# Kernel tuning notes

Hardware: AMD Instinct MI355X
Metric: run time of the kernel (lower is better)

Reference implementation:

```python
import jax, jax.numpy as jnp
import numpy as np
import math

EMB_DIM = 1024
N_HEADS = 16
HEAD_DIM = EMB_DIM // N_HEADS
B, T = 4, 2048


def bitlinear(x, w):
    # BitNet b1.58 absmean ternary quantization. NOTE: the source never
    # rescales the ternary weights by `scale`, so forward uses raw {-1,0,1}.
    scale = jnp.maximum(jnp.mean(jnp.abs(w)), 1e-8)
    w_ternary = jnp.clip(jnp.round(w / scale), -1.0, 1.0)
    w_q = w + jax.lax.stop_gradient(w_ternary - w)  # STE
    return x @ w_q.T


def setup_inputs() -> dict:
    key = jax.random.key(0)
    k1, k2, k3 = jax.random.split(key, 3)
    x = jax.random.normal(k1, (B, T, EMB_DIM), dtype=jnp.float32)
    w_qkv = jax.random.normal(k2, (3 * EMB_DIM, EMB_DIM), dtype=jnp.float32) * 0.02
    w_out = jax.random.normal(k3, (EMB_DIM, EMB_DIM), dtype=jnp.float32) * 0.02
    return {"x": x, "w_qkv": w_qkv, "w_out": w_out}


def reference(x, w_qkv, w_out):
    Bc, Tc, C = x.shape
    qkv = bitlinear(x, w_qkv)  # [B, T, 3C]
    q, k, v = jnp.split(qkv, 3, axis=2)

    def split_heads(t):  # [B, T, C] -> [B, H, T, D]
        return t.reshape(Bc, Tc, N_HEADS, HEAD_DIM).transpose(0, 2, 1, 3)

    q, k, v = split_heads(q), split_heads(k), split_heads(v)
    scale = math.sqrt(HEAD_DIM)
    scores = jnp.einsum("bhqd,bhkd->bhqk", q, k) / scale  # [B, H, T, T]
    causal = jnp.triu(jnp.ones((Tc, Tc), dtype=bool), k=1)
    scores = jnp.where(causal, -jnp.inf, scores)
    attn = jax.nn.softmax(scores, axis=-1)
    out = jnp.einsum("bhqk,bhkd->bhqd", attn, v)  # [B, H, T, D]
    out = out.transpose(0, 2, 1, 3).reshape(Bc, Tc, C)
    return bitlinear(out, w_out)
```

## Files before the change

kernel.cpp:

```cpp
#include <hip/hip_runtime.h>
#include <hip/hip_bf16.h>

#define EMB   1024
#define NHEAD 16
#define HDIM  64
#define BSZ   4
#define SEQ   2048
#define MROWS (BSZ*SEQ)
#define NQKV  (3*EMB)

typedef __bf16 bf16;
typedef __bf16 bf16v4 __attribute__((ext_vector_type(4)));
typedef __bf16 bf16v8 __attribute__((ext_vector_type(8)));
typedef float  f32v4  __attribute__((ext_vector_type(4)));
typedef int    i32v4  __attribute__((ext_vector_type(4)));

#define MFMA16(a,b,c)  __builtin_amdgcn_mfma_f32_16x16x32_bf16((a),(b),(c),0,0,0)
#define MFMAI8(a,b,c)  __builtin_amdgcn_mfma_i32_16x16x64_i8((a),(b),(c),0,0,0)

__device__ __forceinline__ void gload_lds16(const void* g, void* l) {
  __builtin_amdgcn_global_load_lds((const __attribute__((address_space(1))) void*)g,
                                   (__attribute__((address_space(3))) void*)l,
                                   16, 0, 0);
}

#define DPP_FMAX(x, ctrl) do {                                                     \
    int _t = __builtin_amdgcn_update_dpp(0, __float_as_int(x), (ctrl), 0xf, 0xf, true); \
    (x) = fmaxf((x), __int_as_float(_t)); } while (0)


__global__ void zero2_kernel(float* p) { p[threadIdx.x] = 0.f; }

__global__ void abs_sum_kernel(const float* __restrict__ w, int n, float* out) {
  float s = 0.f;
  for (int i = blockIdx.x * blockDim.x + threadIdx.x; i < n; i += gridDim.x * blockDim.x)
    s += fabsf(w[i]);
  #pragma unroll
  for (int off = 32; off; off >>= 1) s += __shfl_down(s, off, 64);
  __shared__ float red[4];
  int lane = threadIdx.x & 63, wid = threadIdx.x >> 6;
  if (lane == 0) red[wid] = s;
  __syncthreads();
  if (threadIdx.x == 0) atomicAdd(out, red[0] + red[1] + red[2] + red[3]);
}

__global__ void ternarize_i8_kernel(const float* __restrict__ w, int n,
                                    const float* __restrict__ sum, char* __restrict__ out) {
  int i = blockIdx.x * blockDim.x + threadIdx.x;
  if (i >= n) return;
  float scale = fmaxf(*sum / (float)n, 1e-8f);
  float t = rintf(w[i] / scale);
  t = fmaxf(-1.f, fminf(1.f, t));
  out[i] = (char)(int)t;
}

__global__ void ternarize_bf16_kernel(const float* __restrict__ w, int n,
                                      const float* __restrict__ sum, bf16* __restrict__ out) {
  int i = blockIdx.x * blockDim.x + threadIdx.x;
  if (i >= n) return;
  float scale = fmaxf(*sum / (float)n, 1e-8f);
  float t = rintf(w[i] / scale);
  t = fmaxf(-1.f, fminf(1.f, t));
  out[i] = (bf16)t;
}

__global__ void quant_x_kernel(const float* __restrict__ x, char* __restrict__ p1,
                               char* __restrict__ p2, int n) {
  int i = blockIdx.x * blockDim.x + threadIdx.x;
  if (i >= n) return;
  float v = x[i];
  float q1 = fminf(fmaxf(rintf(v * 16.f), -127.f), 127.f);
  float r = v - q1 * 0.0625f;
  float q2 = fminf(fmaxf(rintf(r * 4096.f), -127.f), 127.f);
  p1[i] = (char)(int)q1;
  p2[i] = (char)(int)q2;
}


__launch_bounds__(256, 2)
__global__ void gemm_qkv_kernel(const char* __restrict__ xq1, const char* __restrict__ xq2,
                                const char* __restrict__ w8,
                                bf16* __restrict__ qh, bf16* __restrict__ ql,
                                bf16* __restrict__ kh, bf16* __restrict__ kl,
                                bf16* __restrict__ vt) {
  __shared__ __align__(16) char A1[128 * 64];
  __shared__ __align__(16) char A2[128 * 64];
  __shared__ __align__(16) char Bs[128 * 64];
  const int tid = threadIdx.x;
  const int lane = tid & 63, wid = tid >> 6;
  const int quad = lane >> 4, l16 = lane & 15;
  const int m0 = blockIdx.x * 128, n0 = blockIdx.y * 128;
  const int wm = (wid >> 1) * 64, wn = (wid & 1) * 64;
  const int asw = (l16 >> 1) & 3;
  i32v4 acc1[4][4] = {};
  i32v4 acc2[4][4] = {};

  for (int kt = 0; kt < EMB / 64; ++kt) {
    __syncthreads();
    #pragma unroll
    for (int r = 0; r < 2; ++r) {
      int li = r * 256 + tid;
      int row = li >> 2, cs = li & 3;
      int cg = cs ^ ((row >> 1) & 3);
      gload_lds16(xq1 + (size_t)(m0 + row) * EMB + kt * 64 + cg * 16, &A1[li * 16]);
      gload_lds16(xq2 + (size_t)(m0 + row) * EMB + kt * 64 + cg * 16, &A2[li * 16]);
      gload_lds16(w8  + (size_t)(n0 + row) * EMB + kt * 64 + cg * 16, &Bs[li * 16]);
    }
    __syncthreads();
    i32v4 af1[4], af2[4], bfr[4];
    #pragma unroll
    for (int i = 0; i < 4; ++i) {
      int arow = wm + i * 16 + l16;
      int off = arow * 64 + ((quad ^ asw) * 16);
      af1[i] = *(const i32v4*)&A1[off];
      af2[i] = *(const i32v4*)&A2[off];
      int brow = wn + i * 16 + l16;
      bfr[i] = *(const i32v4*)&Bs[brow * 64 + ((quad ^ asw) * 16)];
    }
    #pragma unroll
    for (int i = 0; i < 4; ++i)
      #pragma unroll
      for (int j = 0; j < 4; ++j) {
        acc1[i][j] = MFMAI8(af1[i], bfr[j], acc1[i][j]);
        acc2[i][j] = MFMAI8(af2[i], bfr[j], acc2[i][j]);
      }
  }
  const float S1 = 0.0625f, S2 = 1.f / 4096.f;
  const float QSCALE = 0.18033688011112042f;
  #pragma unroll
  for (int i = 0; i < 4; ++i)
    #pragma unroll
    for (int j = 0; j < 4; ++j) {
      const int n = n0 + wn + j * 16 + l16;
      const int region = n >> 10, c1 = n & 1023, h = c1 >> 6, d = c1 & 63;
      const int m_b = m0 + wm + i * 16 + quad * 4;
      float c[4];
      #pragma unroll
      for (int r = 0; r < 4; ++r)
        c[r] = (float)acc1[i][j][r] * S1 + (float)acc2[i][j][r] * S2;
      if (region == 0) {
        #pragma unroll
        for (int r = 0; r < 4; ++r) {
          int m = m_b + r;
          int b = m >> 11, t = m & (SEQ - 1);
          size_t idx = (((size_t)(b * NHEAD + h) * SEQ + t) << 6) + d;
          float cs = c[r] * QSCALE;
          bf16 hi = (bf16)cs;
          qh[idx] = hi; ql[idx] = (bf16)(cs - (float)hi);
        }
      } else if (region == 1) {
        #pragma unroll
        for (int r = 0; r < 4; ++r) {
          int m = m_b + r;
          int b = m >> 11, t = m & (SEQ - 1);
          size_t idx = (((size_t)(b * NHEAD + h) * SEQ + t) << 6) + d;
          bf16 hi = (bf16)c[r];
          kh[idx] = hi; kl[idx] = (bf16)(c[r] - (float)hi);
        }
      } else {
        bf16v4 pk;
        #pragma unroll
        for (int r = 0; r < 4; ++r) pk[r] = (bf16)c[r];
        int b = m_b >> 11, t = m_b & (SEQ - 1);
        *(bf16v4*)&vt[((size_t)(b * NHEAD + h) * HDIM + d) * SEQ + t] = pk;
      }
    }
}


__launch_bounds__(256, 2)
__global__ void attn_kernel(const bf16* __restrict__ qh, const bf16* __restrict__ ql,
                            const bf16* __restrict__ kh, const bf16* __restrict__ kl,
                            const bf16* __restrict__ vt, bf16* __restrict__ o) {
  __shared__ __align__(16) char smem[66560];
  bf16* Qh = (bf16*)smem;
  bf16* Ql = (bf16*)(smem + 16384);
  bf16* Pw = (bf16*)(smem + 49152);
  const int tid = threadIdx.x;
  const int lane = tid & 63, wid = tid >> 6;
  const int quad = lane >> 4, l16 = lane & 15;
  const int xs = l16 & 7;
  const int pair = blockIdx.x;
  const int bh = blockIdx.y;
  const size_t base = (size_t)bh * SEQ * HDIM;

  auto stage_kv = [&](char* dst, int k0) {
    #pragma unroll
    for (int r = 0; r < 2; ++r) {
      int li = r * 256 + tid;
      int srow = li >> 3, scg = (li & 7) ^ (srow & 7);
      gload_lds16(kh + base + (size_t)(k0 + srow) * HDIM + scg * 8, (bf16*)dst + (size_t)li * 8);
      gload_lds16(kl + base + (size_t)(k0 + srow) * HDIM + scg * 8, (bf16*)(dst + 8192) + (size_t)li * 8);
      gload_lds16(vt + base + (size_t)srow * SEQ + k0 + scg * 8,    (bf16*)(dst + 16384) + (size_t)li * 8);
    }
  };

  bf16v8 ones_f;
  {
    bf16 v1 = (l16 == 0) ? (bf16)1.0f : (bf16)0.0f;
    #pragma unroll
    for (int j = 0; j < 8; ++j) ones_f[j] = v1;
  }
  const int b = bh >> 4, h = bh & 15;

  for (int phase = 0; phase < 2; ++phase) {
    const int qt = phase ? (7 - pair) : (8 + pair);
    const int q0 = qt * 128;

    __syncthreads();
    #pragma unroll
    for (int r = 0; r < 4; ++r) {
      int li = r * 256 + tid;
      int row = li >> 3, cg = (li & 7) ^ (row & 7);
      gload_lds16(qh + base + (size_t)(q0 + row) * HDIM + cg * 8, &Qh[li * 8]);
      gload_lds16(ql + base + (size_t)(q0 + row) * HDIM + cg * 8, &Ql[li * 8]);
    }
    __syncthreads();
    bf16v8 qhf[2][2], qlf[2][2];
    #pragma unroll
    for (int sub = 0; sub < 2; ++sub)
      #pragma unroll
      for (int kk = 0; kk < 2; ++kk) {
        int off = (wid * 32 + sub * 16 + l16) * 64 + (((kk << 2) | quad) ^ xs) * 8;
        qhf[sub][kk] = *(const bf16v8*)&Qh[off];
        qlf[sub][kk] = *(const bf16v8*)&Ql[off];
      }
    __syncthreads();

    f32v4 oacc[2][4] = {};
    f32v4 lacc[2] = {};
    float mrow[2][4];
    #pragma unroll
    for (int s = 0; s < 2; ++s)
      #pragma unroll
      for (int r = 0; r < 4; ++r) mrow[s][r] = -1e30f;

    const int qw0 = q0 + wid * 32;
    const int qrow_hi = qw0 + 31;
    const int ntiles = 2 * qt + 2;

    stage_kv(smem, 0);

    for (int ktile = 0; ktile < ntiles; ++ktile) {
      char* cb = smem + (size_t)((ktile & 1) * 24576);
      char* nb = smem + (size_t)(((ktile + 1) & 1) * 24576);
      __syncthreads();
      if (ktile + 1 < ntiles) stage_kv(nb, (ktile + 1) * 64);
      const int k0 = ktile * 64;
      if (k0 > qrow_hi) continue;

      bf16* Kh_ = (bf16*)cb;
      bf16* Kl_ = (bf16*)(cb + 8192);
      bf16* Vt_ = (bf16*)(cb + 16384);

      f32v4 sacc[2][4] = {};
      #pragma unroll
      for (int kk = 0; kk < 2; ++kk) {
        const int co = (((kk << 2) | quad) ^ xs) * 8;
        bf16v8 khf[4], klf[4];
        #pragma unroll
        for (int nt = 0; nt < 4; ++nt) {
          khf[nt] = *(const bf16v8*)&Kh_[(nt * 16 + l16) * 64 + co];
          klf[nt] = *(const bf16v8*)&Kl_[(nt * 16 + l16) * 64 + co];
        }
        #pragma unroll
        for (int sub = 0; sub < 2; ++sub)
          #pragma unroll
          for (int nt = 0; nt < 4; ++nt) {
            sacc[sub][nt] = MFMA16(qhf[sub][kk], khf[nt], sacc[sub][nt]);
            sacc[sub][nt] = MFMA16(qhf[sub][kk], klf[nt], sacc[sub][nt]);
            sacc[sub][nt] = MFMA16(qlf[sub][kk], khf[nt], sacc[sub][nt]);
          }
      }

      #pragma unroll
      for (int sub = 0; sub < 2; ++sub) {
        if (k0 > qw0 + sub * 16 + 15) continue;
        const int qrow_base = qw0 + sub * 16 + quad * 4;
        #pragma unroll
        for (int nt = 0; nt < 4; ++nt) {
          int key = k0 + nt * 16 + l16;
          #pragma unroll
          for (int r = 0; r < 4; ++r)
            if (key > qrow_base + r) sacc[sub][nt][r] = -1e30f;
        }
        float alpha[4];
        #pragma unroll
        for (int r = 0; r < 4; ++r) {
          float mx = fmaxf(fmaxf(sacc[sub][0][r], sacc[sub][1][r]),
                           fmaxf(sacc[sub][2][r], sacc[sub][3][r]));
          DPP_FMAX(mx, 0x128);
          DPP_FMAX(mx, 0x124);
          DPP_FMAX(mx, 0x122);
          DPP_FMAX(mx, 0x121);
          float mnew = fmaxf(mrow[sub][r], mx);
          alpha[r] = __builtin_amdgcn_exp2f(mrow[sub][r] - mnew);
          mrow[sub][r] = mnew;
        }
        bf16* pwave = Pw + (wid * 2 + sub) * (16 * 68);
        #pragma unroll
        for (int nt = 0; nt < 4; ++nt)
          #pragma unroll
          for (int r = 0; r < 4; ++r)
            pwave[(quad * 4 + r) * 68 + nt * 16 + l16] =
                (bf16)__builtin_amdgcn_exp2f(sacc[sub][nt][r] - mrow[sub][r]);
        #pragma unroll
        for (int r = 0; r < 4; ++r) {
          lacc[sub][r] *= alpha[r];
          #pragma unroll
          for (int dt = 0; dt < 4; ++dt) oacc[sub][dt][r] *= alpha[r];
        }
      }

      #pragma unroll
      for (int kk = 0; kk < 2; ++kk) {
        const int co = (((kk << 2) | quad) ^ xs) * 8;
        bf16v8 vf[4];
        #pragma unroll
        for (int dt = 0; dt < 4; ++dt)
          vf[dt] = *(const bf16v8*)&Vt_[(dt * 16 + l16) * 64 + co];
        #pragma unroll
        for (int sub = 0; sub < 2; ++sub) {
          if (k0 > qw0 + sub * 16 + 15) continue;
          bf16v8 pf = *(const bf16v8*)&Pw[(wid * 2 + sub) * (16 * 68) + l16 * 68 + kk * 32 + quad * 8];
          lacc[sub] = MFMA16(pf, ones_f, lacc[sub]);
          #pragma unroll
          for (int dt = 0; dt < 4; ++dt)
            oacc[sub][dt] = MFMA16(pf, vf[dt], oacc[sub][dt]);
        }
      }
    }

    #pragma unroll
    for (int sub = 0; sub < 2; ++sub) {
      float lrow[4];
      #pragma unroll
      for (int r = 0; r < 4; ++r) lrow[r] = __shfl(lacc[sub][r], lane & 48, 64);
      #pragma unroll
      for (int dt = 0; dt < 4; ++dt)
        #pragma unroll
        for (int r = 0; r < 4; ++r) {
          int q = q0 + wid * 32 + sub * 16 + quad * 4 + r;
          int d = dt * 16 + l16;
          float val = oacc[sub][dt][r] / lrow[r];
          o[((size_t)(b * SEQ + q)) * EMB + h * HDIM + d] = (bf16)val;
        }
    }
  }
}


__launch_bounds__(256, 2)
__global__ void gemm_out_kernel(const bf16* __restrict__ oin, const bf16* __restrict__ wt,
                                float* __restrict__ out) {
  __shared__ __align__(16) bf16 As_[128 * 64];
  __shared__ __align__(16) bf16 Bs_[128 * 64];
  const int tid = threadIdx.x;
  const int lane = tid & 63, wid = tid >> 6;
  const int quad = lane >> 4, l16 = lane & 15;
  const int m0 = blockIdx.x * 128, n0 = blockIdx.y * 128;
  const int wm = (wid >> 1) * 64, wn = (wid & 1) * 64;
  f32v4 acc[4][4] = {};

  for (int kt = 0; kt < EMB / 64; ++kt) {
    __syncthreads();
    #pragma unroll
    for (int r = 0; r < 4; ++r) {
      int li = r * 256 + tid;
      int row = li >> 3, col = (li & 7) * 8;
      gload_lds16(oin + (size_t)(m0 + row) * EMB + kt * 64 + col, &As_[li * 8]);
      gload_lds16(wt  + (size_t)(n0 + row) * EMB + kt * 64 + col, &Bs_[li * 8]);
    }
    __syncthreads();
    #pragma unroll
    for (int kk = 0; kk < 2; ++kk) {
      bf16v8 af[4], bfr[4];
      #pragma unroll
      for (int i = 0; i < 4; ++i) {
        af[i]  = *(const bf16v8*)&As_[(wm + i * 16 + l16) * 64 + kk * 32 + quad * 8];
        bfr[i] = *(const bf16v8*)&Bs_[(wn + i * 16 + l16) * 64 + kk * 32 + quad * 8];
      }
      #pragma unroll
      for (int i = 0; i < 4; ++i)
        #pragma unroll
        for (int j = 0; j < 4; ++j)
          acc[i][j] = MFMA16(af[i], bfr[j], acc[i][j]);
    }
  }
  #pragma unroll
  for (int i = 0; i < 4; ++i)
    #pragma unroll
    for (int j = 0; j < 4; ++j)
      #pragma unroll
      for (int r = 0; r < 4; ++r) {
        int m = m0 + wm + i * 16 + quad * 4 + r;
        int n = n0 + wn + j * 16 + l16;
        out[(size_t)m * EMB + n] = acc[i][j][r];
      }
}


extern "C" void kernel_launch(void* const* d_in, const int* in_sizes, int n_in,
                              void* d_out, int out_size, void* d_ws, size_t ws_size,
                              hipStream_t stream) {
  const float* x     = (const float*)d_in[0];
  const float* w_qkv = (const float*)d_in[1];
  const float* w_out = (const float*)d_in[2];
  float* out = (float*)d_out;
  char* ws = (char*)d_ws;

  const size_t SZ  = (size_t)MROWS * EMB * sizeof(bf16);
  const size_t SZ8 = (size_t)MROWS * EMB;
  size_t off = 0;
  float* sums = (float*)ws;            off = 256;
  char*  wq8  = (char*)(ws + off);     off += (size_t)NQKV * EMB;
  bf16*  wo_t = (bf16*)(ws + off);     off += (size_t)EMB * EMB * sizeof(bf16);
  char*  xq1  = (char*)(ws + off);     off += SZ8;
  char*  xq2  = (char*)(ws + off);     off += SZ8;
  bf16*  qh   = (bf16*)(ws + off);     off += SZ;
  bf16*  ql   = (bf16*)(ws + off);     off += SZ;
  bf16*  kh   = (bf16*)(ws + off);     off += SZ;
  bf16*  kl   = (bf16*)(ws + off);     off += SZ;
  bf16*  vt   = (bf16*)(ws + off);     off += SZ;
  bf16*  ob   = (bf16*)xq1;
  (void)in_sizes; (void)n_in; (void)out_size; (void)ws_size;

  zero2_kernel<<<1, 2, 0, stream>>>(sums);
  abs_sum_kernel<<<256, 256, 0, stream>>>(w_qkv, NQKV * EMB, &sums[0]);
  abs_sum_kernel<<<256, 256, 0, stream>>>(w_out, EMB * EMB, &sums[1]);
  ternarize_i8_kernel<<<(NQKV * EMB) / 256, 256, 0, stream>>>(w_qkv, NQKV * EMB, &sums[0], wq8);
  ternarize_bf16_kernel<<<(EMB * EMB) / 256, 256, 0, stream>>>(w_out, EMB * EMB, &sums[1], wo_t);
  quant_x_kernel<<<(MROWS * EMB) / 256, 256, 0, stream>>>(x, xq1, xq2, MROWS * EMB);
  gemm_qkv_kernel<<<dim3(MROWS / 128, NQKV / 128), 256, 0, stream>>>(xq1, xq2, wq8, qh, ql, kh, kl, vt);
  attn_kernel<<<dim3(8, BSZ * NHEAD), 256, 0, stream>>>(qh, ql, kh, kl, vt, ob);
  gemm_out_kernel<<<dim3(MROWS / 128, EMB / 128), 256, 0, stream>>>(ob, wo_t, out);
}
```

Before: 336.8 us.

## Switch GEMMs to 32x32 MFMA tiles, swizzle out-GEMM LDS, merge ternarize kernels

Both projection GEMMs move from 16x16 MFMA fragments to 32x32 MFMA instructions (i8 32x32x32 for QKV, bf16 32x32x16 for the output), with epilogues remapped to the 32x32 accumulator layout. The output GEMM gets an XOR swizzle on its LDS tiles to reduce bank conflicts. The two ternarize kernels are merged into one launch and the zeroing kernel is replaced by hipMemsetAsync. The aim is fewer MFMA issues and LDS reads per tile and less launch overhead. The trade-off is larger accumulator vectors that raise register pressure and store patterns that may coalesce less well.

```diff
diff --git a/kernel.cpp b/kernel.cpp
--- a/kernel.cpp
+++ b/kernel.cpp
@@ -13,10 +13,13 @@
 typedef __bf16 bf16v4 __attribute__((ext_vector_type(4)));
 typedef __bf16 bf16v8 __attribute__((ext_vector_type(8)));
 typedef float  f32v4  __attribute__((ext_vector_type(4)));
+typedef float  f32v16 __attribute__((ext_vector_type(16)));
 typedef int    i32v4  __attribute__((ext_vector_type(4)));
-
-#define MFMA16(a,b,c)  __builtin_amdgcn_mfma_f32_16x16x32_bf16((a),(b),(c),0,0,0)
-#define MFMAI8(a,b,c)  __builtin_amdgcn_mfma_i32_16x16x64_i8((a),(b),(c),0,0,0)
+typedef int    i32v16 __attribute__((ext_vector_type(16)));
+
+#define MFMA16(a,b,c)   __builtin_amdgcn_mfma_f32_16x16x32_bf16((a),(b),(c),0,0,0)
+#define MFMA32B(a,b,c)  __builtin_amdgcn_mfma_f32_32x32x16_bf16((a),(b),(c),0,0,0)
+#define MFMAI8_32(a,b,c) __builtin_amdgcn_mfma_i32_32x32x32_i8((a),(b),(c),0,0,0)
 
 __device__ __forceinline__ void gload_lds16(const void* g, void* l) {
   __builtin_amdgcn_global_load_lds((const __attribute__((address_space(1))) void*)g,
@@ -28,8 +31,6 @@
     int _t = __builtin_amdgcn_update_dpp(0, __float_as_int(x), (ctrl), 0xf, 0xf, true); \
     (x) = fmaxf((x), __int_as_float(_t)); } while (0)
 
-
-__global__ void zero2_kernel(float* p) { p[threadIdx.x] = 0.f; }
 
 __global__ void abs_sum_kernel(const float* __restrict__ w, int n, float* out) {
   float s = 0.f;
@@ -44,24 +45,23 @@
   if (threadIdx.x == 0) atomicAdd(out, red[0] + red[1] + red[2] + red[3]);
 }
 
-__global__ void ternarize_i8_kernel(const float* __restrict__ w, int n,
-                                    const float* __restrict__ sum, char* __restrict__ out) {
+__global__ void ternarize_both_kernel(const float* __restrict__ wqkv,
+                                      const float* __restrict__ wout,
+                                      const float* __restrict__ sums,
+                                      char* __restrict__ out8,
+                                      bf16* __restrict__ outb) {
   int i = blockIdx.x * blockDim.x + threadIdx.x;
-  if (i >= n) return;
-  float scale = fmaxf(*sum / (float)n, 1e-8f);
-  float t = rintf(w[i] / scale);
-  t = fmaxf(-1.f, fminf(1.f, t));
-  out[i] = (char)(int)t;
-}
-
-__global__ void ternarize_bf16_kernel(const float* __restrict__ w, int n,
-                                      const float* __restrict__ sum, bf16* __restrict__ out) {
-  int i = blockIdx.x * blockDim.x + threadIdx.x;
-  if (i >= n) return;
-  float scale = fmaxf(*sum / (float)n, 1e-8f);
-  float t = rintf(w[i] / scale);
-  t = fmaxf(-1.f, fminf(1.f, t));
-  out[i] = (bf16)t;
+  const int N1 = NQKV * EMB;
+  if (i < N1) {
+    float scale = fmaxf(sums[0] / (float)N1, 1e-8f);
+    float t = rintf(wqkv[i] / scale);
+    out8[i] = (char)(int)fmaxf(-1.f, fminf(1.f, t));
+  } else {
+    int j = i - N1;
+    float scale = fmaxf(sums[1] / (float)(EMB * EMB), 1e-8f);
+    float t = rintf(wout[j] / scale);
+    outb[j] = (bf16)fmaxf(-1.f, fminf(1.f, t));
+  }
 }
 
 __global__ void quant_x_kernel(const float* __restrict__ x, char* __restrict__ p1,
@@ -88,12 +88,11 @@
   __shared__ __align__(16) char Bs[128 * 64];
   const int tid = threadIdx.x;
   const int lane = tid & 63, wid = tid >> 6;
-  const int quad = lane >> 4, l16 = lane & 15;
+  const int c31 = lane & 31, half = lane >> 5;
   const int m0 = blockIdx.x * 128, n0 = blockIdx.y * 128;
   const int wm = (wid >> 1) * 64, wn = (wid & 1) * 64;
-  const int asw = (l16 >> 1) & 3;
-  i32v4 acc1[4][4] = {};
-  i32v4 acc2[4][4] = {};
+  i32v16 acc1[2][2] = {};
+  i32v16 acc2[2][2] = {};
 
   for (int kt = 0; kt < EMB / 64; ++kt) {
     __syncthreads();
@@ -107,62 +106,70 @@
       gload_lds16(w8  + (size_t)(n0 + row) * EMB + kt * 64 + cg * 16, &Bs[li * 16]);
     }
     __syncthreads();
-    i32v4 af1[4], af2[4], bfr[4];
-    #pragma unroll
-    for (int i = 0; i < 4; ++i) {
-      int arow = wm + i * 16 + l16;
-      int off = arow * 64 + ((quad ^ asw) * 16);
-      af1[i] = *(const i32v4*)&A1[off];
-      af2[i] = *(const i32v4*)&A2[off];
-      int brow = wn + i * 16 + l16;
-      bfr[i] = *(const i32v4*)&Bs[brow * 64 + ((quad ^ asw) * 16)];
-    }
-    #pragma unroll
-    for (int i = 0; i < 4; ++i)
-      #pragma unroll
-      for (int j = 0; j < 4; ++j) {
-        acc1[i][j] = MFMAI8(af1[i], bfr[j], acc1[i][j]);
-        acc2[i][j] = MFMAI8(af2[i], bfr[j], acc2[i][j]);
-      }
+    i32v4 a1[2][2], a2[2][2], bq[2][2];
+    #pragma unroll
+    for (int ks = 0; ks < 2; ++ks)
+      #pragma unroll
+      for (int tt = 0; tt < 2; ++tt) {
+        int arow = wm + tt * 32 + c31;
+        int aslot = (ks * 2 + half) ^ ((arow >> 1) & 3);
+        a1[ks][tt] = *(const i32v4*)&A1[arow * 64 + aslot * 16];
+        a2[ks][tt] = *(const i32v4*)&A2[arow * 64 + aslot * 16];
+        int brow = wn + tt * 32 + c31;
+        int bslot = (ks * 2 + half) ^ ((brow >> 1) & 3);
+        bq[ks][tt] = *(const i32v4*)&Bs[brow * 64 + bslot * 16];
+      }
+    #pragma unroll
+    for (int ks = 0; ks < 2; ++ks)
+      #pragma unroll
+      for (int ti = 0; ti < 2; ++ti)
+        #pragma unroll
+        for (int tj = 0; tj < 2; ++tj) {
+          acc1[ti][tj] = MFMAI8_32(a1[ks][ti], bq[ks][tj], acc1[ti][tj]);
+          acc2[ti][tj] = MFMAI8_32(a2[ks][ti], bq[ks][tj], acc2[ti][tj]);
+        }
   }
   const float S1 = 0.0625f, S2 = 1.f / 4096.f;
   const float QSCALE = 0.18033688011112042f;
   #pragma unroll
-  for (int i = 0; i < 4; ++i)
-    #pragma unroll
-    for (int j = 0; j < 4; ++j) {
-      const int n = n0 + wn + j * 16 + l16;
+  for (int ti = 0; ti < 2; ++ti)
+    #pragma unroll
+    for (int tj = 0; tj < 2; ++tj) {
+      const int n = n0 + wn + tj * 32 + c31;
       const int region = n >> 10, c1 = n & 1023, h = c1 >> 6, d = c1 & 63;
-      const int m_b = m0 + wm + i * 16 + quad * 4;
-      float c[4];
-      #pragma unroll
-      for (int r = 0; r < 4; ++r)
-        c[r] = (float)acc1[i][j][r] * S1 + (float)acc2[i][j][r] * S2;
-      if (region == 0) {
-        #pragma unroll
-        for (int r = 0; r < 4; ++r) {
-          int m = m_b + r;
-          int b = m >> 11, t = m & (SEQ - 1);
-          size_t idx = (((size_t)(b * NHEAD + h) * SEQ + t) << 6) + d;
-          float cs = c[r] * QSCALE;
-          bf16 hi = (bf16)cs;
-          qh[idx] = hi; ql[idx] = (bf16)(cs - (float)hi);
-        }
-      } else if (region == 1) {
-        #pragma unroll
-        for (int r = 0; r < 4; ++r) {
-          int m = m_b + r;
-          int b = m >> 11, t = m & (SEQ - 1);
-          size_t idx = (((size_t)(b * NHEAD + h) * SEQ + t) << 6) + d;
-          bf16 hi = (bf16)c[r];
-          kh[idx] = hi; kl[idx] = (bf16)(c[r] - (float)hi);
-        }
-      } else {
-        bf16v4 pk;
-        #pragma unroll
-        for (int r = 0; r < 4; ++r) pk[r] = (bf16)c[r];
-        int b = m_b >> 11, t = m_b & (SEQ - 1);
-        *(bf16v4*)&vt[((size_t)(b * NHEAD + h) * HDIM + d) * SEQ + t] = pk;
+      #pragma unroll
+      for (int g = 0; g < 4; ++g) {
+        const int m_b = m0 + wm + ti * 32 + 8 * g + 4 * half;
+        float c[4];
+        #pragma unroll
+        for (int rr = 0; rr < 4; ++rr)
+          c[rr] = (float)acc1[ti][tj][g * 4 + rr] * S1 + (float)acc2[ti][tj][g * 4 + rr] * S2;
+        if (region == 0) {
+          #pragma unroll
+          for (int rr = 0; rr < 4; ++rr) {
+            int m = m_b + rr;
+            int b = m >> 11, t = m & (SEQ - 1);
+            size_t idx = (((size_t)(b * NHEAD + h) * SEQ + t) << 6) + d;
+            float cs = c[rr] * QSCALE;
+            bf16 hi = (bf16)cs;
+            qh[idx] = hi; ql[idx] = (bf16)(cs - (float)hi);
+          }
+        } else if (region == 1) {
+          #pragma unroll
+          for (int rr = 0; rr < 4; ++rr) {
+            int m = m_b + rr;
+            int b = m >> 11, t = m & (SEQ - 1);
+            size_t idx = (((size_t)(b * NHEAD + h) * SEQ + t) << 6) + d;
+            bf16 hi = (bf16)c[rr];
+            kh[idx] = hi; kl[idx] = (bf16)(c[rr] - (float)hi);
+          }
+        } else {
+          bf16v4 pk;
+          #pragma unroll
+          for (int rr = 0; rr < 4; ++rr) pk[rr] = (bf16)c[rr];
+          int b = m_b >> 11, t = m_b & (SEQ - 1);
+          *(bf16v4*)&vt[((size_t)(b * NHEAD + h) * HDIM + d) * SEQ + t] = pk;
+        }
       }
     }
 }
@@ -357,46 +364,55 @@
   __shared__ __align__(16) bf16 Bs_[128 * 64];
   const int tid = threadIdx.x;
   const int lane = tid & 63, wid = tid >> 6;
-  const int quad = lane >> 4, l16 = lane & 15;
+  const int c31 = lane & 31, half = lane >> 5;
   const int m0 = blockIdx.x * 128, n0 = blockIdx.y * 128;
   const int wm = (wid >> 1) * 64, wn = (wid & 1) * 64;
-  f32v4 acc[4][4] = {};
+  f32v16 acc[2][2] = {};
 
   for (int kt = 0; kt < EMB / 64; ++kt) {
     __syncthreads();
     #pragma unroll
     for (int r = 0; r < 4; ++r) {
       int li = r * 256 + tid;
-      int row = li >> 3, col = (li & 7) * 8;
-      gload_lds16(oin + (size_t)(m0 + row) * EMB + kt * 64 + col, &As_[li * 8]);
-      gload_lds16(wt  + (size_t)(n0 + row) * EMB + kt * 64 + col, &Bs_[li * 8]);
-    }
-    __syncthreads();
-    #pragma unroll
-    for (int kk = 0; kk < 2; ++kk) {
-      bf16v8 af[4], bfr[4];
-      #pragma unroll
-      for (int i = 0; i < 4; ++i) {
-        af[i]  = *(const bf16v8*)&As_[(wm + i * 16 + l16) * 64 + kk * 32 + quad * 8];
-        bfr[i] = *(const bf16v8*)&Bs_[(wn + i * 16 + l16) * 64 + kk * 32 + quad * 8];
-      }
-      #pragma unroll
-      for (int i = 0; i < 4; ++i)
-        #pragma unroll
-        for (int j = 0; j < 4; ++j)
-          acc[i][j] = MFMA16(af[i], bfr[j], acc[i][j]);
-    }
+      int row = li >> 3, cs = li & 7;
+      int cg = cs ^ (row & 7);
+      gload_lds16(oin + (size_t)(m0 + row) * EMB + kt * 64 + cg * 8, &As_[li * 8]);
+      gload_lds16(wt  + (size_t)(n0 + row) * EMB + kt * 64 + cg * 8, &Bs_[li * 8]);
+    }
+    __syncthreads();
+    bf16v8 af[4][2], bq[4][2];
+    #pragma unroll
+    for (int ks = 0; ks < 4; ++ks)
+      #pragma unroll
+      for (int tt = 0; tt < 2; ++tt) {
+        int arow = wm + tt * 32 + c31;
+        int aslot = (2 * ks + half) ^ (arow & 7);
+        af[ks][tt] = *(const bf16v8*)&As_[arow * 64 + aslot * 8];
+        int brow = wn + tt * 32 + c31;
+        int bslot = (2 * ks + half) ^ (brow & 7);
+        bq[ks][tt] = *(const bf16v8*)&Bs_[brow * 64 + bslot * 8];
+      }
+    #pragma unroll
+    for (int ks = 0; ks < 4; ++ks)
+      #pragma unroll
+      for (int ti = 0; ti < 2; ++ti)
+        #pragma unroll
+        for (int tj = 0; tj < 2; ++tj)
+          acc[ti][tj] = MFMA32B(af[ks][ti], bq[ks][tj], acc[ti][tj]);
   }
   #pragma unroll
-  for (int i = 0; i < 4; ++i)
-    #pragma unroll
-    for (int j = 0; j < 4; ++j)
-      #pragma unroll
-      for (int r = 0; r < 4; ++r) {
-        int m = m0 + wm + i * 16 + quad * 4 + r;
-        int n = n0 + wn + j * 16 + l16;
-        out[(size_t)m * EMB + n] = acc[i][j][r];
-      }
+  for (int ti = 0; ti < 2; ++ti)
+    #pragma unroll
+    for (int tj = 0; tj < 2; ++tj) {
+      const int n = n0 + wn + tj * 32 + c31;
+      #pragma unroll
+      for (int g = 0; g < 4; ++g) {
+        const int m_b = m0 + wm + ti * 32 + 8 * g + 4 * half;
+        #pragma unroll
+        for (int rr = 0; rr < 4; ++rr)
+          out[(size_t)(m_b + rr) * EMB + n] = acc[ti][tj][g * 4 + rr];
+      }
+    }
 }
 
 
@@ -425,11 +441,10 @@
   bf16*  ob   = (bf16*)xq1;
   (void)in_sizes; (void)n_in; (void)out_size; (void)ws_size;
 
-  zero2_kernel<<<1, 2, 0, stream>>>(sums);
+  hipMemsetAsync(sums, 0, 2 * sizeof(float), stream);
   abs_sum_kernel<<<256, 256, 0, stream>>>(w_qkv, NQKV * EMB, &sums[0]);
   abs_sum_kernel<<<256, 256, 0, stream>>>(w_out, EMB * EMB, &sums[1]);
-  ternarize_i8_kernel<<<(NQKV * EMB) / 256, 256, 0, stream>>>(w_qkv, NQKV * EMB, &sums[0], wq8);
-  ternarize_bf16_kernel<<<(EMB * EMB) / 256, 256, 0, stream>>>(w_out, EMB * EMB, &sums[1], wo_t);
+  ternarize_both_kernel<<<(NQKV * EMB + EMB * EMB) / 256, 256, 0, stream>>>(w_qkv, w_out, sums, wq8, wo_t);
   quant_x_kernel<<<(MROWS * EMB) / 256, 256, 0, stream>>>(x, xq1, xq2, MROWS * EMB);
   gemm_qkv_kernel<<<dim3(MROWS / 128, NQKV / 128), 256, 0, stream>>>(xq1, xq2, wq8, qh, ql, kh, kl, vt);
   attn_kernel<<<dim3(8, BSZ * NHEAD), 256, 0, stream>>>(qh, ql, kh, kl, vt, ob);
```

Result: no change. 336.9 us (+0.0%).
